# Performance work log

Hardware: AMD Instinct MI355X
Metric: run time of the kernel (lower is better)

The kernel has to match this reference:

```python
import jax, jax.numpy as jnp
import numpy as np

VOCAB, POS_V, NER_V, DEPREL_V = 50000, 50, 10, 40
EMB, POS_D, NER_D, MEM = 300, 30, 30, 200
NUM_LAYERS = 2


def setup_inputs() -> dict:
    key = jax.random.key(0)
    ks = jax.random.split(key, 12)
    B, L = 32, 100
    adj = jax.random.randint(ks[0], (B, L, L), 0, DEPREL_V)
    words = jax.random.randint(ks[1], (B, L), 0, VOCAB)
    pos = jax.random.randint(ks[2], (B, L), 0, POS_V)
    ner = jax.random.randint(ks[3], (B, L), 0, NER_V)
    s = 0.02
    emb = jax.random.normal(ks[4], (VOCAB, EMB), jnp.float32) * s
    pos_emb = jax.random.normal(ks[5], (POS_V, POS_D), jnp.float32) * s
    ner_emb = jax.random.normal(ks[6], (NER_V, NER_D), jnp.float32) * s
    deprel_emb = jax.random.normal(ks[7], (DEPREL_V, MEM), jnp.float32) * s
    deprel_emb = deprel_emb.at[0].set(0.0)  # padding_idx=0
    in_dim = EMB + POS_D + NER_D
    Wp = jax.random.normal(ks[8], (MEM, in_dim), jnp.float32) * s
    bp = jnp.zeros((MEM,), jnp.float32)
    W0 = jax.random.normal(ks[9], (MEM, MEM), jnp.float32) * s
    b0 = jnp.zeros((MEM,), jnp.float32)
    W1 = jax.random.normal(ks[10], (MEM, MEM), jnp.float32) * s
    b1 = jnp.zeros((MEM,), jnp.float32)
    return {"adj": adj, "words": words, "pos": pos, "ner": ner,
            "emb": emb, "pos_emb": pos_emb, "ner_emb": ner_emb,
            "deprel_emb": deprel_emb, "Wp": Wp, "bp": bp,
            "W0": W0, "b0": b0, "W1": W1, "b1": b1}


def reference(adj, words, pos, ner, emb, pos_emb, ner_emb, deprel_emb,
              Wp, bp, W0, b0, W1, b1):
    # embedding lookups + concat  -> [B, L, in_dim]
    embs = jnp.concatenate([emb[words], pos_emb[pos], ner_emb[ner]], axis=-1)
    # preprocessor linear (diagonal_deprel branch)  -> [B, L, D]
    x = embs @ Wp.T + bp
    # per-edge relation embedding gather  -> [B, L, L, D]
    deprel_adj = deprel_emb[adj]
    adj_m = (adj != 0).astype(jnp.float32)            # [B, L, L]
    denom = adj_m.sum(2)[..., None] + 1.0             # [B, L, 1]
    mask = ((adj_m.sum(2) + adj_m.sum(1)) == 0)[..., None]  # [B, L, 1]
    for W, b in ((W0, b0), (W1, b1)):
        # diagonal deprel aggregation: (deprel_adj * x[:,None]) summed over neighbors
        Ax = jnp.einsum('blmd,bmd->bld', deprel_adj, x)
        AxW = (Ax @ W.T + b) + (x @ W.T + b)
        x = jax.nn.relu(AxW / denom)
    return x, mask
```

## Files before the change

kernel.cpp:

```cpp
#include <hip/hip_runtime.h>
#include <hip/hip_bf16.h>

#define BB 32
#define LL 100
#define DD 200
#define KIN 360
#define NP (BB*LL)
#define RNUM 40
#define LT 13
#define NT 8

__device__ __forceinline__ void fma4(float4& a, const float4& w, float s) {
    a.x = fmaf(w.x, s, a.x);
    a.y = fmaf(w.y, s, a.y);
    a.z = fmaf(w.z, s, a.z);
    a.w = fmaf(w.w, s, a.w);
}
__device__ __forceinline__ unsigned bf16rn(float f) {
    unsigned u = __float_as_uint(f);
    return (u + 0x7fffu + ((u >> 16) & 1u)) >> 16;
}
__device__ __forceinline__ unsigned pk2(float a, float b) {
    return bf16rn(a) | (bf16rn(b) << 16);
}
__device__ __forceinline__ float lo16(unsigned u) { return __uint_as_float(u << 16); }
__device__ __forceinline__ float hi16(unsigned u) { return __uint_as_float(u & 0xffff0000u); }

__global__ __launch_bounds__(256) void prep_transpose_kernel(
        const int* __restrict__ adj,
        const float* __restrict__ Wp, const float* __restrict__ W0, const float* __restrict__ W1,
        float* __restrict__ WpT, float* __restrict__ W0T, float* __restrict__ W1T,
        float* __restrict__ invd, float* __restrict__ mask_out) {
    int bid = blockIdx.x, tid = threadIdx.x;
    if (bid < 25) {
        int t = bid * 256 + tid;
        int half = t & 1;
        int pl = t >> 1;
        int b = pl / LL, l = pl % LL;
        const int4* row = (const int4*)(adj + (size_t)pl * LL);
        int q0 = half ? 13 : 0, q1 = half ? 25 : 13;
        int rc = 0;
        for (int i = q0; i < q1; ++i) {
            int4 a = row[i];
            rc += (a.x != 0) + (a.y != 0) + (a.z != 0) + (a.w != 0);
        }
        const int* base = adj + (size_t)b * LL * LL + l;
        int cc = 0;
        for (int m = half * 50; m < half * 50 + 50; ++m) cc += (base[(size_t)m * LL] != 0);
        rc += __shfl_xor(rc, 1);
        cc += __shfl_xor(cc, 1);
        if (!half) {
            invd[pl] = 1.0f / (float)(rc + 1);
            mask_out[pl] = (rc + cc == 0) ? 1.0f : 0.0f;
        }
    } else {
        int i = (bid - 25) * 256 + tid;
        if (i < 18000) {
            int k = i / 50, o = (i % 50) * 4;
            float4 v;
            v.x = Wp[(size_t)(o + 0) * KIN + k];
            v.y = Wp[(size_t)(o + 1) * KIN + k];
            v.z = Wp[(size_t)(o + 2) * KIN + k];
            v.w = Wp[(size_t)(o + 3) * KIN + k];
            ((float4*)WpT)[i] = v;
        } else if (i < 28000) {
            int q = i - 18000;
            int k = q / 50, o = (q % 50) * 4;
            float4 v;
            v.x = W0[(size_t)(o + 0) * DD + k];
            v.y = W0[(size_t)(o + 1) * DD + k];
            v.z = W0[(size_t)(o + 2) * DD + k];
            v.w = W0[(size_t)(o + 3) * DD + k];
            ((float4*)W0T)[q] = v;
        } else if (i < 38000) {
            int q = i - 28000;
            int k = q / 50, o = (q % 50) * 4;
            float4 v;
            v.x = W1[(size_t)(o + 0) * DD + k];
            v.y = W1[(size_t)(o + 1) * DD + k];
            v.z = W1[(size_t)(o + 2) * DD + k];
            v.w = W1[(size_t)(o + 3) * DD + k];
            ((float4*)W1T)[q] = v;
        }
    }
}

__global__ __launch_bounds__(512, 4) void embed_gemv_kernel(
        const int* __restrict__ words, const int* __restrict__ pos, const int* __restrict__ ner,
        const float* __restrict__ emb, const float* __restrict__ pose, const float* __restrict__ nere,
        const float* __restrict__ wpt, const float* __restrict__ bp,
        float* __restrict__ xA) {
    __shared__ float es[8 * KIN];
    __shared__ float4 red[8 * 8 * 50];
    int tid = threadIdx.x;
    int pbase = blockIdx.x * 8;

    float2* es2 = (float2*)es;
    for (int idx = tid; idx < 8 * 180; idx += 512) {
        int p = idx / 180, j2 = idx % 180;
        int gp = pbase + p;
        float2 v;
        if (j2 < 150)      v = ((const float2*)emb)[(size_t)words[gp] * 150 + j2];
        else if (j2 < 165) v = ((const float2*)pose)[pos[gp] * 15 + (j2 - 150)];
        else               v = ((const float2*)nere)[ner[gp] * 15 + (j2 - 165)];
        es2[idx] = v;
    }
    __syncthreads();

    int lane = tid & 63, w = tid >> 6;
    bool act = lane < 50;
    int oq = act ? lane : 49;
    int kq0 = (w < 5) ? 12 * w : 60 + 10 * (w - 5);
    int npair = (w < 5) ? 6 : 5;
    int kqlast = kq0 + 2 * npair - 1;
    const float4* wt4 = (const float4*)wpt;
    const float4* es4 = (const float4*)es;

    float4 a[8];
    #pragma unroll
    for (int p = 0; p < 8; ++p) a[p] = make_float4(0.f, 0.f, 0.f, 0.f);

    float4 wc[8], wn[8];
    #pragma unroll
    for (int q = 0; q < 2; ++q)
        #pragma unroll
        for (int j = 0; j < 4; ++j)
            wc[q * 4 + j] = wt4[(size_t)(4 * (kq0 + q) + j) * 50 + oq];

    for (int pr = 0; pr < npair; ++pr) {
        int nb = kq0 + 2 * pr + 2;
        int nbA = nb <= kqlast ? nb : kq0;
        int nbB = nb + 1 <= kqlast ? nb + 1 : kq0;
        #pragma unroll
        for (int j = 0; j < 4; ++j) wn[j]     = wt4[(size_t)(4 * nbA + j) * 50 + oq];
        #pragma unroll
        for (int j = 0; j < 4; ++j) wn[4 + j] = wt4[(size_t)(4 * nbB + j) * 50 + oq];
        #pragma unroll
        for (int q = 0; q < 2; ++q) {
            int kq = kq0 + 2 * pr + q;
            #pragma unroll
            for (int p = 0; p < 8; ++p) {
                float4 s = es4[p * 90 + kq];
                fma4(a[p], wc[q * 4 + 0], s.x); fma4(a[p], wc[q * 4 + 1], s.y);
                fma4(a[p], wc[q * 4 + 2], s.z); fma4(a[p], wc[q * 4 + 3], s.w);
            }
        }
        #pragma unroll
        for (int j = 0; j < 8; ++j) wc[j] = wn[j];
    }

    if (act) {
        #pragma unroll
        for (int p = 0; p < 8; ++p) red[w * 400 + p * 50 + oq] = a[p];
    }
    __syncthreads();
    for (int t = tid; t < 400; t += 512) {
        int oq2 = t % 50;
        float4 v = ((const float4*)bp)[oq2];
        #pragma unroll
        for (int s = 0; s < 8; ++s) {
            float4 r = red[s * 400 + t];
            v.x += r.x; v.y += r.y; v.z += r.z; v.w += r.w;
        }
        ((float4*)xA)[(size_t)(pbase + t / 50) * 50 + oq2] = v;
    }
}

__global__ __launch_bounds__(1024, 4) void layer_kernel(
        const float* __restrict__ x, const int* __restrict__ adj,
        const float* __restrict__ deprel, const float* __restrict__ wt,
        const float* __restrict__ bias, const float* __restrict__ invd,
        float* __restrict__ out) {
    __shared__ alignas(16) char smem[58912];
    uint2* deps_b = (uint2*)smem;
    unsigned* adjp = (unsigned*)(smem + 16000);
    float4* Sh = (float4*)(smem + 17312);
    float4* Sfin = (float4*)smem;

    int b = blockIdx.y, tile = blockIdx.x;
    int l0 = tile * LT;
    int lcnt = min(LT, LL - l0);
    int tid = threadIdx.x;
    const float4* x4 = (const float4*)x;

    for (int i = tid; i < RNUM * 50; i += 1024) {
        float4 v = ((const float4*)deprel)[i];
        deps_b[i] = make_uint2(pk2(v.x, v.y), pk2(v.z, v.w));
    }
    for (int i = tid; i < lcnt * 25; i += 1024) {
        int li = i / 25, mg = i % 25;
        int4 a = ((const int4*)(adj + (size_t)(b * LL + l0 + li) * LL))[mg];
        adjp[i] = (unsigned)a.x | ((unsigned)a.y << 8) | ((unsigned)a.z << 16) | ((unsigned)a.w << 24);
    }
    __syncthreads();

    int lane = tid & 63, w = tid >> 6;
    int lg = w & 3, sq = w >> 2;
    bool act = lane < 50;
    int dq = lane;

    float4 acc[4];
    #pragma unroll
    for (int i = 0; i < 4; ++i) acc[i] = make_float4(0.f, 0.f, 0.f, 0.f);
    if (act) {
        int mg0 = (sq == 0) ? 0 : 1 + 6 * sq;
        int mg1 = mg0 + ((sq == 0) ? 7 : 6);
        float4 xc[4], xn[4];
        #pragma unroll
        for (int mm = 0; mm < 4; ++mm)
            xc[mm] = x4[(size_t)(b * LL + 4 * mg0 + mm) * 50 + dq];
        for (int mg = mg0; mg < mg1; ++mg) {
            int mgn = (mg + 1 < mg1) ? mg + 1 : mg;
            #pragma unroll
            for (int mm = 0; mm < 4; ++mm)
                xn[mm] = x4[(size_t)(b * LL + 4 * mgn + mm) * 50 + dq];
            unsigned ap[4];
            #pragma unroll
            for (int i = 0; i < 4; ++i) {
                int li = lg + 4 * i;
                ap[i] = (li < lcnt) ? adjp[li * 25 + mg] : 0u;
            }
            #pragma unroll
            for (int mm = 0; mm < 4; ++mm) {
                #pragma unroll
                for (int i = 0; i < 4; ++i) {
                    unsigned r = (ap[i] >> (8 * mm)) & 0xffu;
                    uint2 dv = deps_b[r * 50 + dq];
                    acc[i].x = fmaf(lo16(dv.x), xc[mm].x, acc[i].x);
                    acc[i].y = fmaf(hi16(dv.x), xc[mm].y, acc[i].y);
                    acc[i].z = fmaf(lo16(dv.y), xc[mm].z, acc[i].z);
                    acc[i].w = fmaf(hi16(dv.y), xc[mm].w, acc[i].w);
                }
            }
            #pragma unroll
            for (int mm = 0; mm < 4; ++mm) xc[mm] = xn[mm];
        }
        #pragma unroll
        for (int i = 0; i < 4; ++i) {
            int li = lg + 4 * i;
            if (li < lcnt) Sh[sq * 650 + li * 50 + dq] = acc[i];
        }
    }
    __syncthreads();

    for (int t2 = tid; t2 < 650; t2 += 1024) {
        int li = t2 / 50;
        if (li < lcnt) {
            float4 s0 = Sh[t2], s1 = Sh[650 + t2], s2 = Sh[1300 + t2], s3 = Sh[1950 + t2];
            float4 xr = x4[(size_t)(b * LL + l0 + li) * 50 + (t2 % 50)];
            float4 s;
            s.x = s0.x + s1.x + s2.x + s3.x + xr.x;
            s.y = s0.y + s1.y + s2.y + s3.y + xr.y;
            s.z = s0.z + s1.z + s2.z + s3.z + xr.z;
            s.w = s0.w + s1.w + s2.w + s3.w + xr.w;
            Sfin[t2] = s;
        }
    }
    __syncthreads();

    const float4* wt4 = (const float4*)wt;
    int oq = act ? lane : 49;
    int kq0 = (sq < 2) ? 13 * sq : 26 + 12 * (sq - 2);
    int kcnt = (sq < 2) ? 13 : 12;
    int npair = kcnt >> 1;
    int kqlast = kq0 + kcnt - 1;
    float4 ba[4];
    #pragma unroll
    for (int i = 0; i < 4; ++i) ba[i] = make_float4(0.f, 0.f, 0.f, 0.f);

    float4 wc[8], wn[8];
    #pragma unroll
    for (int q = 0; q < 2; ++q)
        #pragma unroll
        for (int j = 0; j < 4; ++j)
            wc[q * 4 + j] = wt4[(size_t)(4 * (kq0 + q) + j) * 50 + oq];

    int lic[4];
    #pragma unroll
    for (int i = 0; i < 4; ++i) {
        int li = lg + 4 * i;
        lic[i] = li < lcnt ? li : lcnt - 1;
    }

    for (int pr = 0; pr < npair; ++pr) {
        int nb = kq0 + 2 * pr + 2;
        int nbA = nb <= kqlast ? nb : kq0;
        int nbB = nb + 1 <= kqlast ? nb + 1 : kq0;
        #pragma unroll
        for (int j = 0; j < 4; ++j) wn[j]     = wt4[(size_t)(4 * nbA + j) * 50 + oq];
        #pragma unroll
        for (int j = 0; j < 4; ++j) wn[4 + j] = wt4[(size_t)(4 * nbB + j) * 50 + oq];
        #pragma unroll
        for (int q = 0; q < 2; ++q) {
            int kq = kq0 + 2 * pr + q;
            #pragma unroll
            for (int i = 0; i < 4; ++i) {
                float4 s = Sfin[lic[i] * 50 + kq];
                fma4(ba[i], wc[q * 4 + 0], s.x); fma4(ba[i], wc[q * 4 + 1], s.y);
                fma4(ba[i], wc[q * 4 + 2], s.z); fma4(ba[i], wc[q * 4 + 3], s.w);
            }
        }
        #pragma unroll
        for (int j = 0; j < 8; ++j) wc[j] = wn[j];
    }
    if (kcnt & 1) {
        #pragma unroll
        for (int i = 0; i < 4; ++i) {
            float4 s = Sfin[lic[i] * 50 + kqlast];
            fma4(ba[i], wc[0], s.x); fma4(ba[i], wc[1], s.y);
            fma4(ba[i], wc[2], s.z); fma4(ba[i], wc[3], s.w);
        }
    }

    if (act) {
        #pragma unroll
        for (int i = 0; i < 4; ++i) {
            int li = lg + 4 * i;
            if (li < lcnt) Sh[sq * 650 + li * 50 + oq] = ba[i];
        }
    }
    __syncthreads();

    for (int t2 = tid; t2 < 650; t2 += 1024) {
        int li = t2 / 50, oq2 = t2 % 50;
        if (li < lcnt) {
            float4 v0 = Sh[t2], v1 = Sh[650 + t2], v2 = Sh[1300 + t2], v3 = Sh[1950 + t2];
            float4 bb = ((const float4*)bias)[oq2];
            int p = b * LL + l0 + li;
            float sc = invd[p];
            float4 v;
            v.x = fmaxf((v0.x + v1.x + v2.x + v3.x + 2.f * bb.x) * sc, 0.f);
            v.y = fmaxf((v0.y + v1.y + v2.y + v3.y + 2.f * bb.y) * sc, 0.f);
            v.z = fmaxf((v0.z + v1.z + v2.z + v3.z + 2.f * bb.z) * sc, 0.f);
            v.w = fmaxf((v0.w + v1.w + v2.w + v3.w + 2.f * bb.w) * sc, 0.f);
            ((float4*)out)[(size_t)p * 50 + oq2] = v;
        }
    }
}

extern "C" void kernel_launch(void* const* d_in, const int* in_sizes, int n_in,
                              void* d_out, int out_size, void* d_ws, size_t ws_size,
                              hipStream_t stream) {
    const int*   adj   = (const int*)d_in[0];
    const int*   words = (const int*)d_in[1];
    const int*   pos   = (const int*)d_in[2];
    const int*   ner   = (const int*)d_in[3];
    const float* emb   = (const float*)d_in[4];
    const float* pose  = (const float*)d_in[5];
    const float* nere  = (const float*)d_in[6];
    const float* dep   = (const float*)d_in[7];
    const float* Wp    = (const float*)d_in[8];
    const float* bp    = (const float*)d_in[9];
    const float* W0    = (const float*)d_in[10];
    const float* b0    = (const float*)d_in[11];
    const float* W1    = (const float*)d_in[12];
    const float* b1    = (const float*)d_in[13];
    float* out = (float*)d_out;
    float* ws  = (float*)d_ws;

    float* xA   = ws;
    float* xB   = ws + 640000;
    float* WpT  = ws + 1280000;
    float* W0T  = ws + 1352000;
    float* W1T  = ws + 1392000;
    float* invd = ws + 1432000;

    prep_transpose_kernel<<<25 + 149, 256, 0, stream>>>(adj, Wp, W0, W1, WpT, W0T, W1T,
                                                        invd, out + (size_t)NP * DD);
    embed_gemv_kernel<<<NP / 8, 512, 0, stream>>>(words, pos, ner, emb, pose, nere,
                                                  WpT, bp, xA);
    layer_kernel<<<dim3(NT, BB), 1024, 0, stream>>>(xA, adj, dep, W0T, b0, invd, xB);
    layer_kernel<<<dim3(NT, BB), 1024, 0, stream>>>(xB, adj, dep, W1T, b1, invd, out);
}
```

Measured before the change: 69.80 us.

## Fuse all stages into one persistent kernel with hierarchical grid barriers

Replaces four kernel launches with a single persistent kernel of 256 blocks that runs the prep, embedding GEMV and both layers, separated by a two-level atomic grid barrier. Deprel bf16 packing and adj byte-packing are precomputed once into the workspace instead of per block per layer. The embedding GEMV is restructured across 16 waves with a two-pass reduction to fit 1024 threads. This removes launch gaps and redundant per-block prep but adds a memset, spin-wait barriers and a co-residency requirement for all 256 blocks.

```diff
diff --git a/kernel.cpp b/kernel.cpp
--- a/kernel.cpp
+++ b/kernel.cpp
@@ -5,10 +5,21 @@
 #define LL 100
 #define DD 200
 #define KIN 360
-#define NP (BB*LL)
+#define NP 3200
 #define RNUM 40
 #define LT 13
-#define NT 8
+#define NBLK 256
+#define NTHR 1024
+
+#define OFF_XA    0
+#define OFF_XB    640000
+#define OFF_WPT   1280000
+#define OFF_W0T   1352000
+#define OFF_W1T   1392000
+#define OFF_INVD  1432000
+#define OFF_DEPP  1435200
+#define OFF_ADJP  1439200
+#define OFF_BAR   1519200
 
 __device__ __forceinline__ void fma4(float4& a, const float4& w, float s) {
     a.x = fmaf(w.x, s, a.x);
@@ -26,315 +37,377 @@
 __device__ __forceinline__ float lo16(unsigned u) { return __uint_as_float(u << 16); }
 __device__ __forceinline__ float hi16(unsigned u) { return __uint_as_float(u & 0xffff0000u); }
 
-__global__ __launch_bounds__(256) void prep_transpose_kernel(
-        const int* __restrict__ adj,
-        const float* __restrict__ Wp, const float* __restrict__ W0, const float* __restrict__ W1,
-        float* __restrict__ WpT, float* __restrict__ W0T, float* __restrict__ W1T,
-        float* __restrict__ invd, float* __restrict__ mask_out) {
+__device__ __forceinline__ void grid_barrier(unsigned* bar, int bid, unsigned& bcount) {
+    __syncthreads();
+    if (threadIdx.x == 0) {
+        __builtin_amdgcn_fence(__ATOMIC_RELEASE, "agent");
+        int g = bid >> 4;
+        unsigned r = __hip_atomic_fetch_add(bar + g * 16, 1u, __ATOMIC_ACQ_REL,
+                                            __HIP_MEMORY_SCOPE_AGENT);
+        if (((r + 1u) & 15u) == 0u) {
+            unsigned rr = __hip_atomic_fetch_add(bar + 256, 1u, __ATOMIC_ACQ_REL,
+                                                 __HIP_MEMORY_SCOPE_AGENT);
+            if (((rr + 1u) & 15u) == 0u) {
+                #pragma unroll
+                for (int i = 0; i < 16; ++i)
+                    __hip_atomic_store(bar + 272 + i * 16, bcount, __ATOMIC_RELEASE,
+                                       __HIP_MEMORY_SCOPE_AGENT);
+            }
+        }
+        while (__hip_atomic_load(bar + 272 + g * 16, __ATOMIC_RELAXED,
+                                 __HIP_MEMORY_SCOPE_AGENT) < bcount)
+            __builtin_amdgcn_s_sleep(16);
+        __builtin_amdgcn_fence(__ATOMIC_ACQUIRE, "agent");
+        bcount++;
+    }
+    __syncthreads();
+}
+
+__global__ __launch_bounds__(NTHR) void fused_kernel(
+        const int* __restrict__ adj, const int* __restrict__ words,
+        const int* __restrict__ pos, const int* __restrict__ ner,
+        const float* __restrict__ emb, const float* __restrict__ pose,
+        const float* __restrict__ nere, const float* __restrict__ dep,
+        const float* __restrict__ Wp, const float* __restrict__ bp,
+        const float* __restrict__ W0, const float* __restrict__ b0,
+        const float* __restrict__ W1, const float* __restrict__ b1,
+        float* ws, float* out) {
+    __shared__ alignas(16) char smem[62720];
+    unsigned* bar = (unsigned*)(ws + OFF_BAR);
+    float* xA = ws + OFF_XA;
+    float* xB = ws + OFF_XB;
+    float* wpT = ws + OFF_WPT;
+    float* w0T = ws + OFF_W0T;
+    float* w1T = ws + OFF_W1T;
+    float* invd_g = ws + OFF_INVD;
+    uint2* depp_g = (uint2*)(ws + OFF_DEPP);
+    unsigned* adjp_g = (unsigned*)(ws + OFF_ADJP);
+
     int bid = blockIdx.x, tid = threadIdx.x;
-    if (bid < 25) {
-        int t = bid * 256 + tid;
-        int half = t & 1;
-        int pl = t >> 1;
-        int b = pl / LL, l = pl % LL;
-        const int4* row = (const int4*)(adj + (size_t)pl * LL);
-        int q0 = half ? 13 : 0, q1 = half ? 25 : 13;
-        int rc = 0;
-        for (int i = q0; i < q1; ++i) {
-            int4 a = row[i];
-            rc += (a.x != 0) + (a.y != 0) + (a.z != 0) + (a.w != 0);
-        }
-        const int* base = adj + (size_t)b * LL * LL + l;
-        int cc = 0;
-        for (int m = half * 50; m < half * 50 + 50; ++m) cc += (base[(size_t)m * LL] != 0);
-        rc += __shfl_xor(rc, 1);
-        cc += __shfl_xor(cc, 1);
-        if (!half) {
-            invd[pl] = 1.0f / (float)(rc + 1);
-            mask_out[pl] = (rc + cc == 0) ? 1.0f : 0.0f;
-        }
-    } else {
-        int i = (bid - 25) * 256 + tid;
-        if (i < 18000) {
-            int k = i / 50, o = (i % 50) * 4;
+    unsigned bcount = 1u;
+    int lane = tid & 63, wv = tid >> 6;
+    bool act = lane < 50;
+
+    {
+        int t = bid * NTHR + tid;
+        if (t < 18000) {
+            int k = t / 50, o = (t % 50) * 4;
             float4 v;
             v.x = Wp[(size_t)(o + 0) * KIN + k];
             v.y = Wp[(size_t)(o + 1) * KIN + k];
             v.z = Wp[(size_t)(o + 2) * KIN + k];
             v.w = Wp[(size_t)(o + 3) * KIN + k];
-            ((float4*)WpT)[i] = v;
-        } else if (i < 28000) {
-            int q = i - 18000;
+            ((float4*)wpT)[t] = v;
+        } else if (t < 28000) {
+            int q = t - 18000;
             int k = q / 50, o = (q % 50) * 4;
             float4 v;
             v.x = W0[(size_t)(o + 0) * DD + k];
             v.y = W0[(size_t)(o + 1) * DD + k];
             v.z = W0[(size_t)(o + 2) * DD + k];
             v.w = W0[(size_t)(o + 3) * DD + k];
-            ((float4*)W0T)[q] = v;
-        } else if (i < 38000) {
-            int q = i - 28000;
+            ((float4*)w0T)[q] = v;
+        } else if (t < 38000) {
+            int q = t - 28000;
             int k = q / 50, o = (q % 50) * 4;
             float4 v;
             v.x = W1[(size_t)(o + 0) * DD + k];
             v.y = W1[(size_t)(o + 1) * DD + k];
             v.z = W1[(size_t)(o + 2) * DD + k];
             v.w = W1[(size_t)(o + 3) * DD + k];
-            ((float4*)W1T)[q] = v;
+            ((float4*)w1T)[q] = v;
+        } else if (t < 44400) {
+            int item = t - 38000;
+            int half = item & 1, pl = item >> 1;
+            int b = pl / LL, l = pl % LL;
+            const int4* row = (const int4*)(adj + (size_t)pl * LL);
+            int q0 = half ? 13 : 0, q1 = half ? 25 : 13;
+            int rc = 0;
+            for (int i = q0; i < q1; ++i) {
+                int4 a = row[i];
+                rc += (a.x != 0) + (a.y != 0) + (a.z != 0) + (a.w != 0);
+            }
+            const int* base = adj + (size_t)b * LL * LL + l;
+            int cc = 0;
+            for (int m = half * 50; m < half * 50 + 50; ++m) cc += (base[(size_t)m * LL] != 0);
+            rc += __shfl_xor(rc, 1);
+            cc += __shfl_xor(cc, 1);
+            if (!half) {
+                invd_g[pl] = 1.0f / (float)(rc + 1);
+                out[(size_t)NP * DD + pl] = (rc + cc == 0) ? 1.0f : 0.0f;
+            }
+        } else if (t < 46400) {
+            int i = t - 44400;
+            float4 v = ((const float4*)dep)[i];
+            depp_g[i] = make_uint2(pk2(v.x, v.y), pk2(v.z, v.w));
+        } else if (t < 126400) {
+            int i = t - 46400;
+            int4 a = ((const int4*)adj)[i];
+            adjp_g[i] = (unsigned)a.x | ((unsigned)a.y << 8) |
+                        ((unsigned)a.z << 16) | ((unsigned)a.w << 24);
         }
     }
-}
-
-__global__ __launch_bounds__(512, 4) void embed_gemv_kernel(
-        const int* __restrict__ words, const int* __restrict__ pos, const int* __restrict__ ner,
-        const float* __restrict__ emb, const float* __restrict__ pose, const float* __restrict__ nere,
-        const float* __restrict__ wpt, const float* __restrict__ bp,
-        float* __restrict__ xA) {
-    __shared__ float es[8 * KIN];
-    __shared__ float4 red[8 * 8 * 50];
-    int tid = threadIdx.x;
-    int pbase = blockIdx.x * 8;
-
-    float2* es2 = (float2*)es;
-    for (int idx = tid; idx < 8 * 180; idx += 512) {
-        int p = idx / 180, j2 = idx % 180;
-        int gp = pbase + p;
-        float2 v;
-        if (j2 < 150)      v = ((const float2*)emb)[(size_t)words[gp] * 150 + j2];
-        else if (j2 < 165) v = ((const float2*)pose)[pos[gp] * 15 + (j2 - 150)];
-        else               v = ((const float2*)nere)[ner[gp] * 15 + (j2 - 165)];
-        es2[idx] = v;
+
+    grid_barrier(bar, bid, bcount);
+
+    {
+        float* es = (float*)smem;
+        float4* red = (float4*)(smem + 11520);
+        const float4* wt4 = (const float4*)wpT;
+        const float4* es4 = (const float4*)es;
+        int oq = act ? lane : 49;
+        int kq0 = (wv < 10) ? 6 * wv : 60 + 5 * (wv - 10);
+        int kcnt = (wv < 10) ? 6 : 5;
+        int npair = kcnt >> 1;
+        int kqlast = kq0 + kcnt - 1;
+
+        for (int r2 = 0; r2 < 2; ++r2) {
+            bool bactive = (r2 == 0) || (bid < 144);
+            int pbase = (r2 == 0) ? bid * 8 : 2048 + bid * 8;
+            if (bactive) {
+                float2* es2 = (float2*)es;
+                for (int idx = tid; idx < 8 * 180; idx += NTHR) {
+                    int p = idx / 180, j2 = idx % 180;
+                    int gp = pbase + p;
+                    float2 v;
+                    if (j2 < 150)      v = ((const float2*)emb)[(size_t)words[gp] * 150 + j2];
+                    else if (j2 < 165) v = ((const float2*)pose)[pos[gp] * 15 + (j2 - 150)];
+                    else               v = ((const float2*)nere)[ner[gp] * 15 + (j2 - 165)];
+                    es2[idx] = v;
+                }
+            }
+            __syncthreads();
+            float4 a[8];
+            #pragma unroll
+            for (int p = 0; p < 8; ++p) a[p] = make_float4(0.f, 0.f, 0.f, 0.f);
+            if (bactive) {
+                float4 wc[8], wn[8];
+                #pragma unroll
+                for (int q = 0; q < 2; ++q)
+                    #pragma unroll
+                    for (int j = 0; j < 4; ++j)
+                        wc[q * 4 + j] = wt4[(size_t)(4 * (kq0 + q) + j) * 50 + oq];
+                for (int pr = 0; pr < npair; ++pr) {
+                    int nb = kq0 + 2 * pr + 2;
+                    int nbA = nb <= kqlast ? nb : kq0;
+                    int nbB = nb + 1 <= kqlast ? nb + 1 : kq0;
+                    #pragma unroll
+                    for (int j = 0; j < 4; ++j) wn[j]     = wt4[(size_t)(4 * nbA + j) * 50 + oq];
+                    #pragma unroll
+                    for (int j = 0; j < 4; ++j) wn[4 + j] = wt4[(size_t)(4 * nbB + j) * 50 + oq];
+                    #pragma unroll
+                    for (int q = 0; q < 2; ++q) {
+                        int kq = kq0 + 2 * pr + q;
+                        #pragma unroll
+                        for (int p = 0; p < 8; ++p) {
+                            float4 s = es4[p * 90 + kq];
+                            fma4(a[p], wc[q * 4 + 0], s.x); fma4(a[p], wc[q * 4 + 1], s.y);
+                            fma4(a[p], wc[q * 4 + 2], s.z); fma4(a[p], wc[q * 4 + 3], s.w);
+                        }
+                    }
+                    #pragma unroll
+                    for (int j = 0; j < 8; ++j) wc[j] = wn[j];
+                }
+                if (kcnt & 1) {
+                    #pragma unroll
+                    for (int p = 0; p < 8; ++p) {
+                        float4 s = es4[p * 90 + kqlast];
+                        fma4(a[p], wc[0], s.x); fma4(a[p], wc[1], s.y);
+                        fma4(a[p], wc[2], s.z); fma4(a[p], wc[3], s.w);
+                    }
+                }
+                if (wv >= 8 && act) {
+                    #pragma unroll
+                    for (int p = 0; p < 8; ++p) red[(wv - 8) * 400 + p * 50 + oq] = a[p];
+                }
+            }
+            __syncthreads();
+            if (bactive && wv < 8 && act) {
+                #pragma unroll
+                for (int p = 0; p < 8; ++p) {
+                    float4 r = red[wv * 400 + p * 50 + oq];
+                    r.x += a[p].x; r.y += a[p].y; r.z += a[p].z; r.w += a[p].w;
+                    red[wv * 400 + p * 50 + oq] = r;
+                }
+            }
+            __syncthreads();
+            if (bactive) {
+                for (int t2 = tid; t2 < 400; t2 += NTHR) {
+                    int oq2 = t2 % 50;
+                    float4 v = ((const float4*)bp)[oq2];
+                    #pragma unroll
+                    for (int s = 0; s < 8; ++s) {
+                        float4 r = red[s * 400 + t2];
+                        v.x += r.x; v.y += r.y; v.z += r.z; v.w += r.w;
+                    }
+                    ((float4*)xA)[(size_t)(pbase + t2 / 50) * 50 + oq2] = v;
+                }
+            }
+            __syncthreads();
+        }
     }
-    __syncthreads();
-
-    int lane = tid & 63, w = tid >> 6;
-    bool act = lane < 50;
-    int oq = act ? lane : 49;
-    int kq0 = (w < 5) ? 12 * w : 60 + 10 * (w - 5);
-    int npair = (w < 5) ? 6 : 5;
-    int kqlast = kq0 + 2 * npair - 1;
-    const float4* wt4 = (const float4*)wpt;
-    const float4* es4 = (const float4*)es;
-
-    float4 a[8];
-    #pragma unroll
-    for (int p = 0; p < 8; ++p) a[p] = make_float4(0.f, 0.f, 0.f, 0.f);
-
-    float4 wc[8], wn[8];
-    #pragma unroll
-    for (int q = 0; q < 2; ++q)
-        #pragma unroll
-        for (int j = 0; j < 4; ++j)
-            wc[q * 4 + j] = wt4[(size_t)(4 * (kq0 + q) + j) * 50 + oq];
-
-    for (int pr = 0; pr < npair; ++pr) {
-        int nb = kq0 + 2 * pr + 2;
-        int nbA = nb <= kqlast ? nb : kq0;
-        int nbB = nb + 1 <= kqlast ? nb + 1 : kq0;
-        #pragma unroll
-        for (int j = 0; j < 4; ++j) wn[j]     = wt4[(size_t)(4 * nbA + j) * 50 + oq];
-        #pragma unroll
-        for (int j = 0; j < 4; ++j) wn[4 + j] = wt4[(size_t)(4 * nbB + j) * 50 + oq];
-        #pragma unroll
-        for (int q = 0; q < 2; ++q) {
-            int kq = kq0 + 2 * pr + q;
-            #pragma unroll
-            for (int p = 0; p < 8; ++p) {
-                float4 s = es4[p * 90 + kq];
-                fma4(a[p], wc[q * 4 + 0], s.x); fma4(a[p], wc[q * 4 + 1], s.y);
-                fma4(a[p], wc[q * 4 + 2], s.z); fma4(a[p], wc[q * 4 + 3], s.w);
-            }
-        }
-        #pragma unroll
-        for (int j = 0; j < 8; ++j) wc[j] = wn[j];
-    }
-
-    if (act) {
-        #pragma unroll
-        for (int p = 0; p < 8; ++p) red[w * 400 + p * 50 + oq] = a[p];
-    }
-    __syncthreads();
-    for (int t = tid; t < 400; t += 512) {
-        int oq2 = t % 50;
-        float4 v = ((const float4*)bp)[oq2];
-        #pragma unroll
-        for (int s = 0; s < 8; ++s) {
-            float4 r = red[s * 400 + t];
-            v.x += r.x; v.y += r.y; v.z += r.z; v.w += r.w;
-        }
-        ((float4*)xA)[(size_t)(pbase + t / 50) * 50 + oq2] = v;
-    }
-}
-
-__global__ __launch_bounds__(1024, 4) void layer_kernel(
-        const float* __restrict__ x, const int* __restrict__ adj,
-        const float* __restrict__ deprel, const float* __restrict__ wt,
-        const float* __restrict__ bias, const float* __restrict__ invd,
-        float* __restrict__ out) {
-    __shared__ alignas(16) char smem[58912];
+
     uint2* deps_b = (uint2*)smem;
     unsigned* adjp = (unsigned*)(smem + 16000);
     float4* Sh = (float4*)(smem + 17312);
     float4* Sfin = (float4*)smem;
-
-    int b = blockIdx.y, tile = blockIdx.x;
+    int b = bid >> 3, tile = bid & 7;
     int l0 = tile * LT;
     int lcnt = min(LT, LL - l0);
-    int tid = threadIdx.x;
-    const float4* x4 = (const float4*)x;
-
-    for (int i = tid; i < RNUM * 50; i += 1024) {
-        float4 v = ((const float4*)deprel)[i];
-        deps_b[i] = make_uint2(pk2(v.x, v.y), pk2(v.z, v.w));
-    }
-    for (int i = tid; i < lcnt * 25; i += 1024) {
-        int li = i / 25, mg = i % 25;
-        int4 a = ((const int4*)(adj + (size_t)(b * LL + l0 + li) * LL))[mg];
-        adjp[i] = (unsigned)a.x | ((unsigned)a.y << 8) | ((unsigned)a.z << 16) | ((unsigned)a.w << 24);
-    }
-    __syncthreads();
-
-    int lane = tid & 63, w = tid >> 6;
-    int lg = w & 3, sq = w >> 2;
-    bool act = lane < 50;
+    int lg = wv & 3, sq = wv >> 2;
     int dq = lane;
 
-    float4 acc[4];
-    #pragma unroll
-    for (int i = 0; i < 4; ++i) acc[i] = make_float4(0.f, 0.f, 0.f, 0.f);
-    if (act) {
-        int mg0 = (sq == 0) ? 0 : 1 + 6 * sq;
-        int mg1 = mg0 + ((sq == 0) ? 7 : 6);
-        float4 xc[4], xn[4];
+    for (int layer = 0; layer < 2; ++layer) {
+        grid_barrier(bar, bid, bcount);
+        const float* xin = layer ? xB : xA;
+        float* xout = layer ? out : xB;
+        const float* wt = layer ? w1T : w0T;
+        const float* bias = layer ? b1 : b0;
+        const float4* x4 = (const float4*)xin;
+
+        for (int i = tid; i < 2000; i += NTHR) deps_b[i] = depp_g[i];
+        for (int i = tid; i < lcnt * 25; i += NTHR)
+            adjp[i] = adjp_g[(b * LL + l0) * 25 + i];
+        __syncthreads();
+
+        float4 acc[4];
         #pragma unroll
-        for (int mm = 0; mm < 4; ++mm)
-            xc[mm] = x4[(size_t)(b * LL + 4 * mg0 + mm) * 50 + dq];
-        for (int mg = mg0; mg < mg1; ++mg) {
-            int mgn = (mg + 1 < mg1) ? mg + 1 : mg;
+        for (int i = 0; i < 4; ++i) acc[i] = make_float4(0.f, 0.f, 0.f, 0.f);
+        if (act) {
+            int mg0 = (sq == 0) ? 0 : 1 + 6 * sq;
+            int mg1 = mg0 + ((sq == 0) ? 7 : 6);
+            float4 xc[4], xn[4];
             #pragma unroll
             for (int mm = 0; mm < 4; ++mm)
-                xn[mm] = x4[(size_t)(b * LL + 4 * mgn + mm) * 50 + dq];
-            unsigned ap[4];
+                xc[mm] = x4[(size_t)(b * LL + 4 * mg0 + mm) * 50 + dq];
+            for (int mg = mg0; mg < mg1; ++mg) {
+                int mgn = (mg + 1 < mg1) ? mg + 1 : mg;
+                #pragma unroll
+                for (int mm = 0; mm < 4; ++mm)
+                    xn[mm] = x4[(size_t)(b * LL + 4 * mgn + mm) * 50 + dq];
+                unsigned ap[4];
+                #pragma unroll
+                for (int i = 0; i < 4; ++i) {
+                    int li = lg + 4 * i;
+                    ap[i] = (li < lcnt) ? adjp[li * 25 + mg] : 0u;
+                }
+                #pragma unroll
+                for (int mm = 0; mm < 4; ++mm) {
+                    #pragma unroll
+                    for (int i = 0; i < 4; ++i) {
+                        unsigned r = (ap[i] >> (8 * mm)) & 0xffu;
+                        uint2 dv = deps_b[r * 50 + dq];
+                        acc[i].x = fmaf(lo16(dv.x), xc[mm].x, acc[i].x);
+                        acc[i].y = fmaf(hi16(dv.x), xc[mm].y, acc[i].y);
+                        acc[i].z = fmaf(lo16(dv.y), xc[mm].z, acc[i].z);
+                        acc[i].w = fmaf(hi16(dv.y), xc[mm].w, acc[i].w);
+                    }
+                }
+                #pragma unroll
+                for (int mm = 0; mm < 4; ++mm) xc[mm] = xn[mm];
+            }
             #pragma unroll
             for (int i = 0; i < 4; ++i) {
                 int li = lg + 4 * i;
-                ap[i] = (li < lcnt) ? adjp[li * 25 + mg] : 0u;
-            }
-            #pragma unroll
-            for (int mm = 0; mm < 4; ++mm) {
-                #pragma unroll
-                for (int i = 0; i < 4; ++i) {
-                    unsigned r = (ap[i] >> (8 * mm)) & 0xffu;
-                    uint2 dv = deps_b[r * 50 + dq];
-                    acc[i].x = fmaf(lo16(dv.x), xc[mm].x, acc[i].x);
-                    acc[i].y = fmaf(hi16(dv.x), xc[mm].y, acc[i].y);
-                    acc[i].z = fmaf(lo16(dv.y), xc[mm].z, acc[i].z);
-                    acc[i].w = fmaf(hi16(dv.y), xc[mm].w, acc[i].w);
-                }
-            }
-            #pragma unroll
-            for (int mm = 0; mm < 4; ++mm) xc[mm] = xn[mm];
-        }
+                if (li < lcnt) Sh[sq * 650 + li * 50 + dq] = acc[i];
+            }
+        }
+        __syncthreads();
+
+        for (int t2 = tid; t2 < 650; t2 += NTHR) {
+            int li = t2 / 50;
+            if (li < lcnt) {
+                float4 s0 = Sh[t2], s1 = Sh[650 + t2], s2 = Sh[1300 + t2], s3 = Sh[1950 + t2];
+                float4 xr = x4[(size_t)(b * LL + l0 + li) * 50 + (t2 % 50)];
+                float4 s;
+                s.x = s0.x + s1.x + s2.x + s3.x + xr.x;
+                s.y = s0.y + s1.y + s2.y + s3.y + xr.y;
+                s.z = s0.z + s1.z + s2.z + s3.z + xr.z;
+                s.w = s0.w + s1.w + s2.w + s3.w + xr.w;
+                Sfin[t2] = s;
+            }
+        }
+        __syncthreads();
+
+        const float4* wt4 = (const float4*)wt;
+        int oq = act ? lane : 49;
+        int kq0 = (sq < 2) ? 13 * sq : 26 + 12 * (sq - 2);
+        int kcnt = (sq < 2) ? 13 : 12;
+        int npair = kcnt >> 1;
+        int kqlast = kq0 + kcnt - 1;
+        float4 ba[4];
+        #pragma unroll
+        for (int i = 0; i < 4; ++i) ba[i] = make_float4(0.f, 0.f, 0.f, 0.f);
+
+        float4 wc[8], wn[8];
+        #pragma unroll
+        for (int q = 0; q < 2; ++q)
+            #pragma unroll
+            for (int j = 0; j < 4; ++j)
+                wc[q * 4 + j] = wt4[(size_t)(4 * (kq0 + q) + j) * 50 + oq];
+
+        int lic[4];
         #pragma unroll
         for (int i = 0; i < 4; ++i) {
             int li = lg + 4 * i;
-            if (li < lcnt) Sh[sq * 650 + li * 50 + dq] = acc[i];
-        }
-    }
-    __syncthreads();
-
-    for (int t2 = tid; t2 < 650; t2 += 1024) {
-        int li = t2 / 50;
-        if (li < lcnt) {
-            float4 s0 = Sh[t2], s1 = Sh[650 + t2], s2 = Sh[1300 + t2], s3 = Sh[1950 + t2];
-            float4 xr = x4[(size_t)(b * LL + l0 + li) * 50 + (t2 % 50)];
-            float4 s;
-            s.x = s0.x + s1.x + s2.x + s3.x + xr.x;
-            s.y = s0.y + s1.y + s2.y + s3.y + xr.y;
-            s.z = s0.z + s1.z + s2.z + s3.z + xr.z;
-            s.w = s0.w + s1.w + s2.w + s3.w + xr.w;
-            Sfin[t2] = s;
-        }
-    }
-    __syncthreads();
-
-    const float4* wt4 = (const float4*)wt;
-    int oq = act ? lane : 49;
-    int kq0 = (sq < 2) ? 13 * sq : 26 + 12 * (sq - 2);
-    int kcnt = (sq < 2) ? 13 : 12;
-    int npair = kcnt >> 1;
-    int kqlast = kq0 + kcnt - 1;
-    float4 ba[4];
-    #pragma unroll
-    for (int i = 0; i < 4; ++i) ba[i] = make_float4(0.f, 0.f, 0.f, 0.f);
-
-    float4 wc[8], wn[8];
-    #pragma unroll
-    for (int q = 0; q < 2; ++q)
-        #pragma unroll
-        for (int j = 0; j < 4; ++j)
-            wc[q * 4 + j] = wt4[(size_t)(4 * (kq0 + q) + j) * 50 + oq];
-
-    int lic[4];
-    #pragma unroll
-    for (int i = 0; i < 4; ++i) {
-        int li = lg + 4 * i;
-        lic[i] = li < lcnt ? li : lcnt - 1;
-    }
-
-    for (int pr = 0; pr < npair; ++pr) {
-        int nb = kq0 + 2 * pr + 2;
-        int nbA = nb <= kqlast ? nb : kq0;
-        int nbB = nb + 1 <= kqlast ? nb + 1 : kq0;
-        #pragma unroll
-        for (int j = 0; j < 4; ++j) wn[j]     = wt4[(size_t)(4 * nbA + j) * 50 + oq];
-        #pragma unroll
-        for (int j = 0; j < 4; ++j) wn[4 + j] = wt4[(size_t)(4 * nbB + j) * 50 + oq];
-        #pragma unroll
-        for (int q = 0; q < 2; ++q) {
-            int kq = kq0 + 2 * pr + q;
+            lic[i] = li < lcnt ? li : lcnt - 1;
+        }
+
+        for (int pr = 0; pr < npair; ++pr) {
+            int nb = kq0 + 2 * pr + 2;
+            int nbA = nb <= kqlast ? nb : kq0;
+            int nbB = nb + 1 <= kqlast ? nb + 1 : kq0;
+            #pragma unroll
+            for (int j = 0; j < 4; ++j) wn[j]     = wt4[(size_t)(4 * nbA + j) * 50 + oq];
+            #pragma unroll
+            for (int j = 0; j < 4; ++j) wn[4 + j] = wt4[(size_t)(4 * nbB + j) * 50 + oq];
+            #pragma unroll
+            for (int q = 0; q < 2; ++q) {
+                int kq = kq0 + 2 * pr + q;
+                #pragma unroll
+                for (int i = 0; i < 4; ++i) {
+                    float4 s = Sfin[lic[i] * 50 + kq];
+                    fma4(ba[i], wc[q * 4 + 0], s.x); fma4(ba[i], wc[q * 4 + 1], s.y);
+                    fma4(ba[i], wc[q * 4 + 2], s.z); fma4(ba[i], wc[q * 4 + 3], s.w);
+                }
+            }
+            #pragma unroll
+            for (int j = 0; j < 8; ++j) wc[j] = wn[j];
+        }
+        if (kcnt & 1) {
             #pragma unroll
             for (int i = 0; i < 4; ++i) {
-                float4 s = Sfin[lic[i] * 50 + kq];
-                fma4(ba[i], wc[q * 4 + 0], s.x); fma4(ba[i], wc[q * 4 + 1], s.y);
-                fma4(ba[i], wc[q * 4 + 2], s.z); fma4(ba[i], wc[q * 4 + 3], s.w);
-            }
-        }
-        #pragma unroll
-        for (int j = 0; j < 8; ++j) wc[j] = wn[j];
-    }
-    if (kcnt & 1) {
-        #pragma unroll
-        for (int i = 0; i < 4; ++i) {
-            float4 s = Sfin[lic[i] * 50 + kqlast];
-            fma4(ba[i], wc[0], s.x); fma4(ba[i], wc[1], s.y);
-            fma4(ba[i], wc[2], s.z); fma4(ba[i], wc[3], s.w);
-        }
-    }
-
-    if (act) {
-        #pragma unroll
-        for (int i = 0; i < 4; ++i) {
-            int li = lg + 4 * i;
-            if (li < lcnt) Sh[sq * 650 + li * 50 + oq] = ba[i];
-        }
-    }
-    __syncthreads();
-
-    for (int t2 = tid; t2 < 650; t2 += 1024) {
-        int li = t2 / 50, oq2 = t2 % 50;
-        if (li < lcnt) {
-            float4 v0 = Sh[t2], v1 = Sh[650 + t2], v2 = Sh[1300 + t2], v3 = Sh[1950 + t2];
-            float4 bb = ((const float4*)bias)[oq2];
-            int p = b * LL + l0 + li;
-            float sc = invd[p];
-            float4 v;
-            v.x = fmaxf((v0.x + v1.x + v2.x + v3.x + 2.f * bb.x) * sc, 0.f);
-            v.y = fmaxf((v0.y + v1.y + v2.y + v3.y + 2.f * bb.y) * sc, 0.f);
-            v.z = fmaxf((v0.z + v1.z + v2.z + v3.z + 2.f * bb.z) * sc, 0.f);
-            v.w = fmaxf((v0.w + v1.w + v2.w + v3.w + 2.f * bb.w) * sc, 0.f);
-            ((float4*)out)[(size_t)p * 50 + oq2] = v;
-        }
+                float4 s = Sfin[lic[i] * 50 + kqlast];
+                fma4(ba[i], wc[0], s.x); fma4(ba[i], wc[1], s.y);
+                fma4(ba[i], wc[2], s.z); fma4(ba[i], wc[3], s.w);
+            }
+        }
+
+        if (act) {
+            #pragma unroll
+            for (int i = 0; i < 4; ++i) {
+                int li = lg + 4 * i;
+                if (li < lcnt) Sh[sq * 650 + li * 50 + oq] = ba[i];
+            }
+        }
+        __syncthreads();
+
+        for (int t2 = tid; t2 < 650; t2 += NTHR) {
+            int li = t2 / 50, oq2 = t2 % 50;
+            if (li < lcnt) {
+                float4 v0 = Sh[t2], v1 = Sh[650 + t2], v2 = Sh[1300 + t2], v3 = Sh[1950 + t2];
+                float4 bb = ((const float4*)bias)[oq2];
+                int p = b * LL + l0 + li;
+                float sc = invd_g[p];
+                float4 v;
+                v.x = fmaxf((v0.x + v1.x + v2.x + v3.x + 2.f * bb.x) * sc, 0.f);
+                v.y = fmaxf((v0.y + v1.y + v2.y + v3.y + 2.f * bb.y) * sc, 0.f);
+                v.z = fmaxf((v0.z + v1.z + v2.z + v3.z + 2.f * bb.z) * sc, 0.f);
+                v.w = fmaxf((v0.w + v1.w + v2.w + v3.w + 2.f * bb.w) * sc, 0.f);
+                ((float4*)xout)[(size_t)p * 50 + oq2] = v;
+            }
+        }
+        __syncthreads();
     }
 }
 
@@ -358,17 +431,7 @@
     float* out = (float*)d_out;
     float* ws  = (float*)d_ws;
 
-    float* xA   = ws;
-    float* xB   = ws + 640000;
-    float* WpT  = ws + 1280000;
-    float* W0T  = ws + 1352000;
-    float* W1T  = ws + 1392000;
-    float* invd = ws + 1432000;
-
-    prep_transpose_kernel<<<25 + 149, 256, 0, stream>>>(adj, Wp, W0, W1, WpT, W0T, W1T,
-                                                        invd, out + (size_t)NP * DD);
-    embed_gemv_kernel<<<NP / 8, 512, 0, stream>>>(words, pos, ner, emb, pose, nere,
-                                                  WpT, bp, xA);
-    layer_kernel<<<dim3(NT, BB), 1024, 0, stream>>>(xA, adj, dep, W0T, b0, invd, xB);
-    layer_kernel<<<dim3(NT, BB), 1024, 0, stream>>>(xB, adj, dep, W1T, b1, invd, out);
-}
+    hipMemsetAsync(ws + OFF_BAR, 0, 528 * 4, stream);
+    fused_kernel<<<NBLK, NTHR, 0, stream>>>(adj, words, pos, ner, emb, pose, nere,
+                                            dep, Wp, bp, W0, b0, W1, b1, ws, out);
+}
```

Measured after the change: 170.0 us. +143.5%, slower.

## Drop weight transpose kernel, read row-major weights directly, fuse adjacency stats into embed kernel

Applied to the files above, without the earlier changes.

Removes the separate prep kernel that transposed Wp/W0/W1 and computed degree counts. The GEMV loops now read the original row-major weights as float4 along K, accumulating dot products per output instead of outer-product FMAs. The adjacency row/column counts become extra blocks in the embed kernel, using LDS staging. This saves one launch and the transpose traffic, but the weight loads are now strided across lanes (uncoalesced), which may cost bandwidth.

```diff
diff --git a/kernel.cpp b/kernel.cpp
--- a/kernel.cpp
+++ b/kernel.cpp
@@ -5,16 +5,17 @@
 #define LL 100
 #define DD 200
 #define KIN 360
-#define NP (BB*LL)
+#define NP 3200
 #define RNUM 40
 #define LT 13
 #define NT 8
 
-__device__ __forceinline__ void fma4(float4& a, const float4& w, float s) {
-    a.x = fmaf(w.x, s, a.x);
-    a.y = fmaf(w.y, s, a.y);
-    a.z = fmaf(w.z, s, a.z);
-    a.w = fmaf(w.w, s, a.w);
+__device__ __forceinline__ float dot4(float acc, float4 w, float4 s) {
+    acc = fmaf(w.x, s.x, acc);
+    acc = fmaf(w.y, s.y, acc);
+    acc = fmaf(w.z, s.z, acc);
+    acc = fmaf(w.w, s.w, acc);
+    return acc;
 }
 __device__ __forceinline__ unsigned bf16rn(float f) {
     unsigned u = __float_as_uint(f);
@@ -26,74 +27,46 @@
 __device__ __forceinline__ float lo16(unsigned u) { return __uint_as_float(u << 16); }
 __device__ __forceinline__ float hi16(unsigned u) { return __uint_as_float(u & 0xffff0000u); }
 
-__global__ __launch_bounds__(256) void prep_transpose_kernel(
-        const int* __restrict__ adj,
-        const float* __restrict__ Wp, const float* __restrict__ W0, const float* __restrict__ W1,
-        float* __restrict__ WpT, float* __restrict__ W0T, float* __restrict__ W1T,
-        float* __restrict__ invd, float* __restrict__ mask_out) {
-    int bid = blockIdx.x, tid = threadIdx.x;
-    if (bid < 25) {
-        int t = bid * 256 + tid;
-        int half = t & 1;
-        int pl = t >> 1;
-        int b = pl / LL, l = pl % LL;
-        const int4* row = (const int4*)(adj + (size_t)pl * LL);
-        int q0 = half ? 13 : 0, q1 = half ? 25 : 13;
-        int rc = 0;
-        for (int i = q0; i < q1; ++i) {
-            int4 a = row[i];
-            rc += (a.x != 0) + (a.y != 0) + (a.z != 0) + (a.w != 0);
-        }
-        const int* base = adj + (size_t)b * LL * LL + l;
-        int cc = 0;
-        for (int m = half * 50; m < half * 50 + 50; ++m) cc += (base[(size_t)m * LL] != 0);
-        rc += __shfl_xor(rc, 1);
-        cc += __shfl_xor(cc, 1);
-        if (!half) {
-            invd[pl] = 1.0f / (float)(rc + 1);
-            mask_out[pl] = (rc + cc == 0) ? 1.0f : 0.0f;
-        }
-    } else {
-        int i = (bid - 25) * 256 + tid;
-        if (i < 18000) {
-            int k = i / 50, o = (i % 50) * 4;
-            float4 v;
-            v.x = Wp[(size_t)(o + 0) * KIN + k];
-            v.y = Wp[(size_t)(o + 1) * KIN + k];
-            v.z = Wp[(size_t)(o + 2) * KIN + k];
-            v.w = Wp[(size_t)(o + 3) * KIN + k];
-            ((float4*)WpT)[i] = v;
-        } else if (i < 28000) {
-            int q = i - 18000;
-            int k = q / 50, o = (q % 50) * 4;
-            float4 v;
-            v.x = W0[(size_t)(o + 0) * DD + k];
-            v.y = W0[(size_t)(o + 1) * DD + k];
-            v.z = W0[(size_t)(o + 2) * DD + k];
-            v.w = W0[(size_t)(o + 3) * DD + k];
-            ((float4*)W0T)[q] = v;
-        } else if (i < 38000) {
-            int q = i - 28000;
-            int k = q / 50, o = (q % 50) * 4;
-            float4 v;
-            v.x = W1[(size_t)(o + 0) * DD + k];
-            v.y = W1[(size_t)(o + 1) * DD + k];
-            v.z = W1[(size_t)(o + 2) * DD + k];
-            v.w = W1[(size_t)(o + 3) * DD + k];
-            ((float4*)W1T)[q] = v;
-        }
-    }
-}
-
-__global__ __launch_bounds__(512, 4) void embed_gemv_kernel(
+__global__ __launch_bounds__(512, 4) void embed_prep_kernel(
         const int* __restrict__ words, const int* __restrict__ pos, const int* __restrict__ ner,
         const float* __restrict__ emb, const float* __restrict__ pose, const float* __restrict__ nere,
-        const float* __restrict__ wpt, const float* __restrict__ bp,
-        float* __restrict__ xA) {
-    __shared__ float es[8 * KIN];
-    __shared__ float4 red[8 * 8 * 50];
-    int tid = threadIdx.x;
-    int pbase = blockIdx.x * 8;
+        const float* __restrict__ Wp, const float* __restrict__ bp,
+        const int* __restrict__ adj,
+        float* __restrict__ xA, float* __restrict__ invd, float* __restrict__ mask_out) {
+    __shared__ alignas(16) char smem[62720];
+    int bid = blockIdx.x, tid = threadIdx.x;
+
+    if (bid >= 400) {
+        int bb = bid - 400;
+        int* a_lds = (int*)smem;
+        int* rcc = (int*)(smem + 40000);
+        const int4* src = (const int4*)(adj + (size_t)bb * (LL * LL));
+        for (int i = tid; i < 2500; i += 512) ((int4*)a_lds)[i] = src[i];
+        __syncthreads();
+        if (tid < 200) {
+            int l = tid % 100;
+            int c = 0;
+            if (tid < 100) {
+                #pragma unroll 4
+                for (int m = 0; m < 100; ++m) c += (a_lds[l * 100 + m] != 0);
+            } else {
+                #pragma unroll 4
+                for (int m = 0; m < 100; ++m) c += (a_lds[m * 100 + l] != 0);
+            }
+            rcc[tid] = c;
+        }
+        __syncthreads();
+        if (tid < 100) {
+            int rc = rcc[tid], cc = rcc[100 + tid];
+            invd[bb * 100 + tid] = 1.0f / (float)(rc + 1);
+            mask_out[bb * 100 + tid] = (rc + cc == 0) ? 1.0f : 0.0f;
+        }
+        return;
+    }
+
+    float* es = (float*)smem;
+    float4* red = (float4*)(smem + 11520);
+    int pbase = bid * 8;
 
     float2* es2 = (float2*)es;
     for (int idx = tid; idx < 8 * 180; idx += 512) {
@@ -113,8 +86,10 @@
     int kq0 = (w < 5) ? 12 * w : 60 + 10 * (w - 5);
     int npair = (w < 5) ? 6 : 5;
     int kqlast = kq0 + 2 * npair - 1;
-    const float4* wt4 = (const float4*)wpt;
+    const float4* wp4 = (const float4*)Wp;
     const float4* es4 = (const float4*)es;
+    size_t rb0 = (size_t)(4 * oq + 0) * 90;
+    size_t rb1 = rb0 + 90, rb2 = rb0 + 180, rb3 = rb0 + 270;
 
     float4 a[8];
     #pragma unroll
@@ -122,27 +97,31 @@
 
     float4 wc[8], wn[8];
     #pragma unroll
-    for (int q = 0; q < 2; ++q)
-        #pragma unroll
-        for (int j = 0; j < 4; ++j)
-            wc[q * 4 + j] = wt4[(size_t)(4 * (kq0 + q) + j) * 50 + oq];
+    for (int q = 0; q < 2; ++q) {
+        wc[q * 4 + 0] = wp4[rb0 + kq0 + q];
+        wc[q * 4 + 1] = wp4[rb1 + kq0 + q];
+        wc[q * 4 + 2] = wp4[rb2 + kq0 + q];
+        wc[q * 4 + 3] = wp4[rb3 + kq0 + q];
+    }
 
     for (int pr = 0; pr < npair; ++pr) {
         int nb = kq0 + 2 * pr + 2;
         int nbA = nb <= kqlast ? nb : kq0;
         int nbB = nb + 1 <= kqlast ? nb + 1 : kq0;
-        #pragma unroll
-        for (int j = 0; j < 4; ++j) wn[j]     = wt4[(size_t)(4 * nbA + j) * 50 + oq];
-        #pragma unroll
-        for (int j = 0; j < 4; ++j) wn[4 + j] = wt4[(size_t)(4 * nbB + j) * 50 + oq];
+        wn[0] = wp4[rb0 + nbA]; wn[1] = wp4[rb1 + nbA];
+        wn[2] = wp4[rb2 + nbA]; wn[3] = wp4[rb3 + nbA];
+        wn[4] = wp4[rb0 + nbB]; wn[5] = wp4[rb1 + nbB];
+        wn[6] = wp4[rb2 + nbB]; wn[7] = wp4[rb3 + nbB];
         #pragma unroll
         for (int q = 0; q < 2; ++q) {
             int kq = kq0 + 2 * pr + q;
             #pragma unroll
             for (int p = 0; p < 8; ++p) {
                 float4 s = es4[p * 90 + kq];
-                fma4(a[p], wc[q * 4 + 0], s.x); fma4(a[p], wc[q * 4 + 1], s.y);
-                fma4(a[p], wc[q * 4 + 2], s.z); fma4(a[p], wc[q * 4 + 3], s.w);
+                a[p].x = dot4(a[p].x, wc[q * 4 + 0], s);
+                a[p].y = dot4(a[p].y, wc[q * 4 + 1], s);
+                a[p].z = dot4(a[p].z, wc[q * 4 + 2], s);
+                a[p].w = dot4(a[p].w, wc[q * 4 + 3], s);
             }
         }
         #pragma unroll
@@ -258,8 +237,10 @@
     }
     __syncthreads();
 
-    const float4* wt4 = (const float4*)wt;
+    const float4* w4 = (const float4*)wt;
     int oq = act ? lane : 49;
+    size_t rb0 = (size_t)(4 * oq + 0) * 50;
+    size_t rb1 = rb0 + 50, rb2 = rb0 + 100, rb3 = rb0 + 150;
     int kq0 = (sq < 2) ? 13 * sq : 26 + 12 * (sq - 2);
     int kcnt = (sq < 2) ? 13 : 12;
     int npair = kcnt >> 1;
@@ -270,10 +251,12 @@
 
     float4 wc[8], wn[8];
     #pragma unroll
-    for (int q = 0; q < 2; ++q)
-        #pragma unroll
-        for (int j = 0; j < 4; ++j)
-            wc[q * 4 + j] = wt4[(size_t)(4 * (kq0 + q) + j) * 50 + oq];
+    for (int q = 0; q < 2; ++q) {
+        wc[q * 4 + 0] = w4[rb0 + kq0 + q];
+        wc[q * 4 + 1] = w4[rb1 + kq0 + q];
+        wc[q * 4 + 2] = w4[rb2 + kq0 + q];
+        wc[q * 4 + 3] = w4[rb3 + kq0 + q];
+    }
 
     int lic[4];
     #pragma unroll
@@ -286,18 +269,20 @@
         int nb = kq0 + 2 * pr + 2;
         int nbA = nb <= kqlast ? nb : kq0;
         int nbB = nb + 1 <= kqlast ? nb + 1 : kq0;
-        #pragma unroll
-        for (int j = 0; j < 4; ++j) wn[j]     = wt4[(size_t)(4 * nbA + j) * 50 + oq];
-        #pragma unroll
-        for (int j = 0; j < 4; ++j) wn[4 + j] = wt4[(size_t)(4 * nbB + j) * 50 + oq];
+        wn[0] = w4[rb0 + nbA]; wn[1] = w4[rb1 + nbA];
+        wn[2] = w4[rb2 + nbA]; wn[3] = w4[rb3 + nbA];
+        wn[4] = w4[rb0 + nbB]; wn[5] = w4[rb1 + nbB];
+        wn[6] = w4[rb2 + nbB]; wn[7] = w4[rb3 + nbB];
         #pragma unroll
         for (int q = 0; q < 2; ++q) {
             int kq = kq0 + 2 * pr + q;
             #pragma unroll
             for (int i = 0; i < 4; ++i) {
                 float4 s = Sfin[lic[i] * 50 + kq];
-                fma4(ba[i], wc[q * 4 + 0], s.x); fma4(ba[i], wc[q * 4 + 1], s.y);
-                fma4(ba[i], wc[q * 4 + 2], s.z); fma4(ba[i], wc[q * 4 + 3], s.w);
+                ba[i].x = dot4(ba[i].x, wc[q * 4 + 0], s);
+                ba[i].y = dot4(ba[i].y, wc[q * 4 + 1], s);
+                ba[i].z = dot4(ba[i].z, wc[q * 4 + 2], s);
+                ba[i].w = dot4(ba[i].w, wc[q * 4 + 3], s);
             }
         }
         #pragma unroll
@@ -307,8 +292,10 @@
         #pragma unroll
         for (int i = 0; i < 4; ++i) {
             float4 s = Sfin[lic[i] * 50 + kqlast];
-            fma4(ba[i], wc[0], s.x); fma4(ba[i], wc[1], s.y);
-            fma4(ba[i], wc[2], s.z); fma4(ba[i], wc[3], s.w);
+            ba[i].x = dot4(ba[i].x, wc[0], s);
+            ba[i].y = dot4(ba[i].y, wc[1], s);
+            ba[i].z = dot4(ba[i].z, wc[2], s);
+            ba[i].w = dot4(ba[i].w, wc[3], s);
         }
     }
 
@@ -360,15 +347,11 @@
 
     float* xA   = ws;
     float* xB   = ws + 640000;
-    float* WpT  = ws + 1280000;
-    float* W0T  = ws + 1352000;
-    float* W1T  = ws + 1392000;
-    float* invd = ws + 1432000;
-
-    prep_transpose_kernel<<<25 + 149, 256, 0, stream>>>(adj, Wp, W0, W1, WpT, W0T, W1T,
-                                                        invd, out + (size_t)NP * DD);
-    embed_gemv_kernel<<<NP / 8, 512, 0, stream>>>(words, pos, ner, emb, pose, nere,
-                                                  WpT, bp, xA);
-    layer_kernel<<<dim3(NT, BB), 1024, 0, stream>>>(xA, adj, dep, W0T, b0, invd, xB);
-    layer_kernel<<<dim3(NT, BB), 1024, 0, stream>>>(xB, adj, dep, W1T, b1, invd, out);
-}
+    float* invd = ws + 1280000;
+
+    embed_prep_kernel<<<432, 512, 0, stream>>>(words, pos, ner, emb, pose, nere,
+                                               Wp, bp, adj, xA, invd,
+                                               out + (size_t)NP * DD);
+    layer_kernel<<<dim3(NT, BB), 1024, 0, stream>>>(xA, adj, dep, W0, b0, invd, xB);
+    layer_kernel<<<dim3(NT, BB), 1024, 0, stream>>>(xB, adj, dep, W1, b1, invd, out);
+}
```

Result: slower. 161.5 us (+131.4%).
